# Kernel optimization log

Measured on AMD Instinct MI355X. Metric: run time of the kernel, lower is better.

The kernel has to match this reference:

```python
import jax, jax.numpy as jnp
import numpy as np

B, S, C, H, F = 4, 2048, 256, 8, 512  # scenes, pillars/scene, embed, heads, ffn hidden
D = C // H


def setup_inputs() -> dict:
    key = jax.random.key(0)
    ks = jax.random.split(key, 6)
    n = lambda k, sh: jax.random.normal(k, sh, jnp.float32) * 0.02
    # batch index sorted, equal-size contiguous segments per scene
    bidx = (jnp.arange(B * S, dtype=jnp.int32) // S)[:, None]
    coords = jnp.concatenate([bidx, jnp.zeros((B * S, 3), jnp.int32)], axis=1)
    return dict(
        pillar_features=jax.random.normal(ks[0], (B * S, C), jnp.float32),
        voxel_coords=coords,
        w_qkv=n(ks[1], (3 * C, C)), b_qkv=jnp.zeros((3 * C,), jnp.float32),
        w_out=n(ks[2], (C, C)), b_out=jnp.zeros((C,), jnp.float32),
        ln1_g=jnp.ones((C,), jnp.float32), ln1_b=jnp.zeros((C,), jnp.float32),
        w1=n(ks[3], (F, C)), b1=jnp.zeros((F,), jnp.float32),
        w2=n(ks[4], (C, F)), b2=jnp.zeros((C,), jnp.float32),
        ln2_g=jnp.ones((C,), jnp.float32), ln2_b=jnp.zeros((C,), jnp.float32),
    )


def _ln(x, g, b):
    m = x.mean(-1, keepdims=True)
    v = x.var(-1, keepdims=True)  # biased var, matches torch LayerNorm
    return (x - m) / jnp.sqrt(v + 1e-5) * g + b


def reference(pillar_features, voxel_coords, w_qkv, b_qkv, w_out, b_out,
              ln1_g, ln1_b, w1, b1, w2, b2, ln2_g, ln2_b):
    # coords[:,0] is sorted with equal-size contiguous segments, so the
    # per-batch mask-gather in the original is exactly a reshape here.
    x = pillar_features.reshape(B, S, C)
    qkv = x @ w_qkv.T + b_qkv                      # [B,S,3C]
    q, k, v = jnp.split(qkv, 3, axis=-1)
    rs = lambda t: t.reshape(B, S, H, D).transpose(0, 2, 1, 3)  # [B,H,S,D]
    q, k, v = rs(q), rs(k), rs(v)
    scores = jnp.einsum('bhqd,bhkd->bhqk', q, k) / jnp.sqrt(jnp.float32(D))
    att = jax.nn.softmax(scores, axis=-1)
    o = jnp.einsum('bhqk,bhkd->bhqd', att, v).transpose(0, 2, 1, 3).reshape(B, S, C)
    o = o @ w_out.T + b_out
    x = _ln(x + o, ln1_g, ln1_b)
    f = jax.nn.gelu(x @ w1.T + b1, approximate=False) @ w2.T + b2
    x = _ln(x + f, ln2_g, ln2_b)
    return x.reshape(B * S, C)
```

## Files before the change

kernel.cpp:

```cpp
#include <hip/hip_runtime.h>
#include <math.h>

#define MROWS 8192
#define BATCH 4
#define SEQ   2048
#define CDIM  256
#define HEADS 8
#define DHEAD 32
#define FDIM  512
#define QKVN  768

typedef __attribute__((ext_vector_type(8))) short bf16x8;
typedef __attribute__((ext_vector_type(4))) float f32x4;

__device__ __forceinline__ unsigned pk_bf16(float a, float b) {
  unsigned r;
  asm("v_cvt_pk_bf16_f32 %0, %1, %2" : "=v"(r) : "v"(a), "v"(b));
  return r;
}
__device__ __forceinline__ float bf2f(short s) {
  unsigned u = ((unsigned)(unsigned short)s) << 16;
  return __builtin_bit_cast(float, u);
}
__device__ __forceinline__ float bflo(unsigned w) {
  return __builtin_bit_cast(float, w << 16);
}
__device__ __forceinline__ float bfhi(unsigned w) {
  return __builtin_bit_cast(float, w & 0xffff0000u);
}
__device__ __forceinline__ short f2bf(float f) {
  unsigned u = __builtin_bit_cast(unsigned, f);
  u = (u + 0x7FFFu + ((u >> 16) & 1u)) >> 16;
  return (short)u;
}
__device__ __forceinline__ float fexp2(float x) {
#if __has_builtin(__builtin_amdgcn_exp2f)
  return __builtin_amdgcn_exp2f(x);
#else
  return exp2f(x);
#endif
}
__device__ __forceinline__ void gl16(const void* g, void* l) {
  __builtin_amdgcn_global_load_lds(
      (const __attribute__((address_space(1))) void*)g,
      (__attribute__((address_space(3))) void*)l, 16, 0, 0);
}
__device__ __forceinline__ float gelu_tanh(float v) {
  const float u = v * (0.7978845608f + 0.0356774081f * v * v);
  const float t = fexp2(u * 2.885390082f);
  return v * t / (t + 1.0f);
}

__global__ __launch_bounds__(256) void cast_all_k(
    const float* __restrict__ pillar, short* __restrict__ pb,
    const float* __restrict__ wq, short* __restrict__ wqb,
    const float* __restrict__ wo, short* __restrict__ wob,
    const float* __restrict__ w1, short* __restrict__ w1b,
    const float* __restrict__ w2, short* __restrict__ w2b)
{
  const int i = blockIdx.x * 256 + threadIdx.x;
  const float* s; short* d; int off;
  if (i < 524288)      { s = pillar; d = pb;  off = i; }
  else if (i < 573440) { s = wq;     d = wqb; off = i - 524288; }
  else if (i < 589824) { s = wo;     d = wob; off = i - 573440; }
  else if (i < 622592) { s = w1;     d = w1b; off = i - 589824; }
  else                 { s = w2;     d = w2b; off = i - 622592; }
  float4 v = reinterpret_cast<const float4*>(s)[off];
  uint2 o = { pk_bf16(v.x, v.y), pk_bf16(v.z, v.w) };
  *reinterpret_cast<uint2*>(d + off*4) = o;
}

template<int K, bool BF16OUT, bool GELU, bool VOUT>
__global__ __launch_bounds__(256) void gemm64_k(
    const short* __restrict__ A, const short* __restrict__ W,
    const float* __restrict__ bias, void* __restrict__ out,
    short* __restrict__ vt, int NS)
{
  __shared__ short AS[2][4096];
  __shared__ short WS[2][4096];
  const int tid = threadIdx.x;
  const int l   = tid & 63;
  const int w   = tid >> 6;
  const int m0 = blockIdx.x * 64;
  const int n0 = blockIdx.y * 64;
  const int wr = (w >> 1) * 32;
  const int wc = (w & 1) * 32;
  const int lr = l & 15;
  const int lg = l >> 4;

  f32x4 acc[2][2];
#pragma unroll
  for (int i = 0; i < 2; ++i)
#pragma unroll
    for (int j = 0; j < 2; ++j) acc[i][j] = (f32x4){0.f,0.f,0.f,0.f};

  auto stage = [&](int buf, int k0) {
#pragma unroll
    for (int i = 0; i < 2; ++i) {
      const int c = i*256 + tid;
      const int r = c >> 3;
      const int s = (c & 7) ^ (r & 7);
      gl16(A + (size_t)(m0 + r)*K + k0 + s*8, &AS[buf][c*8]);
      gl16(W + (size_t)(n0 + r)*K + k0 + s*8, &WS[buf][c*8]);
    }
  };

  stage(0, 0);
  const int NST = K / 64;
  for (int t = 0; t < NST; ++t) {
    const int buf = t & 1;
    __syncthreads();
    if (t + 1 < NST) stage(buf ^ 1, (t+1)*64);
#pragma unroll
    for (int ks = 0; ks < 2; ++ks) {
      const int sl = ((ks*4 + lg) ^ (lr & 7)) << 3;
      bf16x8 a[2], b[2];
#pragma unroll
      for (int mi = 0; mi < 2; ++mi)
        a[mi] = *reinterpret_cast<const bf16x8*>(&AS[buf][(wr + mi*16 + lr)*64 + sl]);
#pragma unroll
      for (int nj = 0; nj < 2; ++nj)
        b[nj] = *reinterpret_cast<const bf16x8*>(&WS[buf][(wc + nj*16 + lr)*64 + sl]);
#pragma unroll
      for (int mi = 0; mi < 2; ++mi)
#pragma unroll
        for (int nj = 0; nj < 2; ++nj)
          acc[mi][nj] = __builtin_amdgcn_mfma_f32_16x16x32_bf16(b[nj], a[mi], acc[mi][nj], 0, 0, 0);
    }
  }

#pragma unroll
  for (int mi = 0; mi < 2; ++mi) {
    const size_t m = m0 + wr + mi*16 + lr;
#pragma unroll
    for (int nj = 0; nj < 2; ++nj) {
      const int nf = n0 + wc + nj*16 + lg*4;
      float4 bs = *reinterpret_cast<const float4*>(&bias[nf]);
      f32x4 v = acc[mi][nj];
      float v0 = v[0]+bs.x, v1 = v[1]+bs.y, v2 = v[2]+bs.z, v3 = v[3]+bs.w;
      if (GELU) { v0 = gelu_tanh(v0); v1 = gelu_tanh(v1); v2 = gelu_tanh(v2); v3 = gelu_tanh(v3); }
      if (VOUT && n0 >= 512) {
        const int nl = nf - 512;
        const int hh = nl >> 5, dvb = nl & 31;
        const int bb = (int)(m >> 11), ss = (int)(m & 2047);
        short* vp = vt + ((size_t)((bb*8 + hh)*32 + dvb))*2048 + ss;
        vp[0] = f2bf(v0); vp[2048] = f2bf(v1); vp[4096] = f2bf(v2); vp[6144] = f2bf(v3);
      } else if (BF16OUT) {
        uint2 p = { pk_bf16(v0, v1), pk_bf16(v2, v3) };
        *reinterpret_cast<uint2*>((short*)out + m*NS + nf) = p;
      } else {
        float4 p = { v0, v1, v2, v3 };
        *reinterpret_cast<float4*>((float*)out + m*NS + nf) = p;
      }
    }
  }
}

__global__ __launch_bounds__(512, 8) void attn_mfma_k(
    const short* __restrict__ qk, const short* __restrict__ vtg,
    short* __restrict__ attno)
{
  __shared__ short KS[2][2][2048];
  __shared__ short VS[2][2][2048];

  const int tid  = threadIdx.x;
  const int lane = tid & 63;
  const int wv   = tid >> 6;
  const int st   = wv >> 2;
  const int qw   = wv & 3;
  const int bh   = blockIdx.y;
  const int b    = bh >> 3, h = bh & 7;
  const int q0   = blockIdx.x * 64 + qw * 16;

  const int lr = lane & 15;
  const int lg = lane >> 4;

  bf16x8 qf;
  {
    bf16x8 qraw = *reinterpret_cast<const bf16x8*>(
        qk + (size_t)(b*SEQ + q0 + lr)*512 + h*DHEAD + lg*8);
    const float c = 0.25508134f;
#pragma unroll
    for (int j = 0; j < 8; ++j) qf[j] = f2bf(bf2f(qraw[j]) * c);
  }
  bf16x8 ones;
#pragma unroll
  for (int j = 0; j < 8; ++j) ones[j] = (short)0x3F80;

  f32x4 o0 = {0.f,0.f,0.f,0.f}, o1 = {0.f,0.f,0.f,0.f};
  f32x4 lacc = {0.f,0.f,0.f,0.f};

  const int t256 = tid & 255;
  const short* kSrc;
  {
    const int r = t256 >> 2, s = t256 & 3;
    const int rr = r & 31;
    const int key = ((rr >> 2) & 3)*8 + ((rr >> 4) & 1)*4 + (rr & 3) + (r & 32);
    const int slog = s ^ ((r >> 1) & 3);
    kSrc = qk + (size_t)(b*SEQ + st*1024 + key)*512 + 256 + h*DHEAD + slog*8;
  }
  const short* vSrc;
  {
    const int r = t256 >> 3, s = t256 & 7;
    const int slog = s ^ (r & 7);
    vSrc = vtg + ((size_t)(bh*32 + r))*2048 + st*1024 + slog*8;
  }

  gl16(kSrc, &KS[st][0][t256*8]);
  gl16(vSrc, &VS[st][0][t256*8]);
  kSrc += 64*512; vSrc += 64;

  const int kxor = (lr >> 1) & 3;
  const int vxor = lr & 7;

  for (int t = 0; t < 16; ++t) {
    const int buf = t & 1;
    __syncthreads();
    if (t + 1 < 16) {
      gl16(kSrc, &KS[st][buf^1][t256*8]);
      gl16(vSrc, &VS[st][buf^1][t256*8]);
      kSrc += 64*512; vSrc += 64;
    }

#pragma unroll
    for (int half = 0; half < 2; ++half) {
      const int krow = (half*32 + lr)*32 + ((lg ^ kxor) << 3);
      bf16x8 kf0 = *reinterpret_cast<const bf16x8*>(&KS[st][buf][krow]);
      bf16x8 kf1 = *reinterpret_cast<const bf16x8*>(&KS[st][buf][krow + 512]);
      f32x4 z = {0.f,0.f,0.f,0.f};
      f32x4 s0 = __builtin_amdgcn_mfma_f32_16x16x32_bf16(kf0, qf, z, 0, 0, 0);
      f32x4 s1 = __builtin_amdgcn_mfma_f32_16x16x32_bf16(kf1, qf, z, 0, 0, 0);

      const int vcol = (((half*4 + lg) ^ vxor) << 3);
      bf16x8 vf0 = *reinterpret_cast<const bf16x8*>(&VS[st][buf][lr*64 + vcol]);
      bf16x8 vf1 = *reinterpret_cast<const bf16x8*>(&VS[st][buf][(lr+16)*64 + vcol]);

      float p0 = fexp2(s0[0]), p1 = fexp2(s0[1]), p2 = fexp2(s0[2]), p3 = fexp2(s0[3]);
      float p4 = fexp2(s1[0]), p5 = fexp2(s1[1]), p6 = fexp2(s1[2]), p7 = fexp2(s1[3]);
      union { bf16x8 v; unsigned w[4]; } pfu;
      pfu.w[0] = pk_bf16(p0, p1); pfu.w[1] = pk_bf16(p2, p3);
      pfu.w[2] = pk_bf16(p4, p5); pfu.w[3] = pk_bf16(p6, p7);

      o0   = __builtin_amdgcn_mfma_f32_16x16x32_bf16(vf0, pfu.v, o0, 0, 0, 0);
      o1   = __builtin_amdgcn_mfma_f32_16x16x32_bf16(vf1, pfu.v, o1, 0, 0, 0);
      lacc = __builtin_amdgcn_mfma_f32_16x16x32_bf16(ones, pfu.v, lacc, 0, 0, 0);
    }
  }

  __syncthreads();
  float* mg = (float*)&KS[0][0][0];
  const int mi = (qw*64 + lane)*10;
  if (st == 1) {
    mg[mi+0]=o0[0]; mg[mi+1]=o0[1]; mg[mi+2]=o0[2]; mg[mi+3]=o0[3];
    mg[mi+4]=o1[0]; mg[mi+5]=o1[1]; mg[mi+6]=o1[2]; mg[mi+7]=o1[3];
    mg[mi+8]=lacc[0];
  }
  __syncthreads();
  if (st == 0) {
    const float inv = 1.f / (lacc[0] + mg[mi+8]);
    float a0 = (o0[0]+mg[mi+0])*inv, a1 = (o0[1]+mg[mi+1])*inv;
    float a2 = (o0[2]+mg[mi+2])*inv, a3 = (o0[3]+mg[mi+3])*inv;
    float b0 = (o1[0]+mg[mi+4])*inv, b1 = (o1[1]+mg[mi+5])*inv;
    float b2 = (o1[2]+mg[mi+6])*inv, b3 = (o1[3]+mg[mi+7])*inv;
    short* op = attno + (size_t)(b*SEQ + q0 + lr)*CDIM + h*DHEAD;
    uint2 r0 = { pk_bf16(a0, a1), pk_bf16(a2, a3) };
    uint2 r1 = { pk_bf16(b0, b1), pk_bf16(b2, b3) };
    *reinterpret_cast<uint2*>(op + lg*4)      = r0;
    *reinterpret_cast<uint2*>(op + 16 + lg*4) = r1;
  }
}

template<int K, bool F32OUT>
__global__ __launch_bounds__(512, 4) void gemmln_k(
    const short* __restrict__ A, const short* __restrict__ W,
    const float* __restrict__ bias, const short* __restrict__ resid,
    const float* __restrict__ g, const float* __restrict__ bta,
    float* __restrict__ outf, short* __restrict__ outb)
{
  __shared__ short AS[2][2048];
  __shared__ short WS[2][16384];
  __shared__ float P[32][4][2];
  const int tid = threadIdx.x;
  const int l   = tid & 63;
  const int wv  = tid >> 6;
  const int wm  = wv >> 2;
  const int wn  = wv & 3;
  const int m0  = blockIdx.x * 32;
  const int lr  = l & 15;
  const int lg  = l >> 4;

  f32x4 acc[4];
#pragma unroll
  for (int j = 0; j < 4; ++j) acc[j] = (f32x4){0.f,0.f,0.f,0.f};

  auto stage = [&](int buf, int k0) {
    if (tid < 256) {
      const int r = tid >> 3;
      const int s = (tid & 7) ^ (r & 7);
      gl16(A + (size_t)(m0 + r)*K + k0 + s*8, &AS[buf][tid*8]);
    }
#pragma unroll
    for (int i = 0; i < 4; ++i) {
      const int c = i*512 + tid;
      const int r = c >> 3;
      const int s = (c & 7) ^ (r & 7);
      gl16(W + (size_t)r*K + k0 + s*8, &WS[buf][c*8]);
    }
  };

  stage(0, 0);
  const int NST = K / 64;
  for (int t = 0; t < NST; ++t) {
    const int buf = t & 1;
    __syncthreads();
    if (t + 1 < NST) stage(buf ^ 1, (t+1)*64);
#pragma unroll
    for (int ks = 0; ks < 2; ++ks) {
      const int sl = ((ks*4 + lg) ^ (lr & 7)) << 3;
      bf16x8 a = *reinterpret_cast<const bf16x8*>(&AS[buf][(wm*16 + lr)*64 + sl]);
#pragma unroll
      for (int nj = 0; nj < 4; ++nj) {
        bf16x8 b = *reinterpret_cast<const bf16x8*>(&WS[buf][(wn*64 + nj*16 + lr)*64 + sl]);
        acc[nj] = __builtin_amdgcn_mfma_f32_16x16x32_bf16(b, a, acc[nj], 0, 0, 0);
      }
    }
  }

  const int m = m0 + wm*16 + lr;
  float vals[16];
  float s = 0.f, sq = 0.f;
#pragma unroll
  for (int nj = 0; nj < 4; ++nj) {
    const int col = wn*64 + nj*16 + lg*4;
    float4 bs = *reinterpret_cast<const float4*>(&bias[col]);
    uint2 rv = *reinterpret_cast<const uint2*>(&resid[(size_t)m*CDIM + col]);
    float v0 = acc[nj][0] + bs.x + bflo(rv.x);
    float v1 = acc[nj][1] + bs.y + bfhi(rv.x);
    float v2 = acc[nj][2] + bs.z + bflo(rv.y);
    float v3 = acc[nj][3] + bs.w + bfhi(rv.y);
    vals[nj*4+0]=v0; vals[nj*4+1]=v1; vals[nj*4+2]=v2; vals[nj*4+3]=v3;
    s += (v0+v1)+(v2+v3);
    sq += (v0*v0+v1*v1)+(v2*v2+v3*v3);
  }
  s  += __shfl_xor(s, 16);  s  += __shfl_xor(s, 32);
  sq += __shfl_xor(sq, 16); sq += __shfl_xor(sq, 32);
  if (lg == 0) { P[wm*16 + lr][wn][0] = s; P[wm*16 + lr][wn][1] = sq; }
  __syncthreads();
  const float S  = P[wm*16+lr][0][0] + P[wm*16+lr][1][0] + P[wm*16+lr][2][0] + P[wm*16+lr][3][0];
  const float SQ = P[wm*16+lr][0][1] + P[wm*16+lr][1][1] + P[wm*16+lr][2][1] + P[wm*16+lr][3][1];
  const float mean = S * (1.f/CDIM);
  const float var  = SQ * (1.f/CDIM) - mean*mean;
  const float rstd = rsqrtf(var + 1e-5f);
#pragma unroll
  for (int nj = 0; nj < 4; ++nj) {
    const int col = wn*64 + nj*16 + lg*4;
    float4 gv = *reinterpret_cast<const float4*>(&g[col]);
    float4 bv = *reinterpret_cast<const float4*>(&bta[col]);
    float r0 = (vals[nj*4+0]-mean)*rstd*gv.x + bv.x;
    float r1 = (vals[nj*4+1]-mean)*rstd*gv.y + bv.y;
    float r2 = (vals[nj*4+2]-mean)*rstd*gv.z + bv.z;
    float r3 = (vals[nj*4+3]-mean)*rstd*gv.w + bv.w;
    if (F32OUT) {
      float4 p = { r0, r1, r2, r3 };
      *reinterpret_cast<float4*>(&outf[(size_t)m*CDIM + col]) = p;
    } else {
      uint2 p = { pk_bf16(r0, r1), pk_bf16(r2, r3) };
      *reinterpret_cast<uint2*>(outb + (size_t)m*CDIM + col) = p;
    }
  }
}

extern "C" void kernel_launch(void* const* d_in, const int* in_sizes, int n_in,
                              void* d_out, int out_size, void* d_ws, size_t ws_size,
                              hipStream_t stream)
{
  const float* pillar = (const float*)d_in[0];
  const float* w_qkv  = (const float*)d_in[2];
  const float* b_qkv  = (const float*)d_in[3];
  const float* w_out  = (const float*)d_in[4];
  const float* b_out  = (const float*)d_in[5];
  const float* ln1_g  = (const float*)d_in[6];
  const float* ln1_b  = (const float*)d_in[7];
  const float* w1     = (const float*)d_in[8];
  const float* b1     = (const float*)d_in[9];
  const float* w2     = (const float*)d_in[10];
  const float* b2     = (const float*)d_in[11];
  const float* ln2_g  = (const float*)d_in[12];
  const float* ln2_b  = (const float*)d_in[13];
  float* out = (float*)d_out;
  short* sb  = (short*)d_ws;

  short* pb    = sb;
  short* wqb   = sb + 2097152;
  short* wob   = sb + 2293760;
  short* w1b   = sb + 2359296;
  short* w2b   = sb + 2490368;
  short* qk    = sb + 2621440;
  short* vtg   = sb + 6815744;
  short* attnb = sb + 8912896;
  short* x1b   = sb + 2621440;
  short* yhidb = sb + 4718592;

  cast_all_k<<<2560, 256, 0, stream>>>(pillar, pb, w_qkv, wqb, w_out, wob,
                                       w1, w1b, w2, w2b);

  gemm64_k<CDIM, true, false, true><<<dim3(MROWS/64, QKVN/64), 256, 0, stream>>>(
      pb, wqb, b_qkv, qk, vtg, 512);

  attn_mfma_k<<<dim3(SEQ/64, BATCH*HEADS), 512, 0, stream>>>(qk, vtg, attnb);

  gemmln_k<CDIM, false><<<dim3(MROWS/32), 512, 0, stream>>>(
      attnb, wob, b_out, pb, ln1_g, ln1_b, nullptr, x1b);

  gemm64_k<CDIM, true, true, false><<<dim3(MROWS/64, FDIM/64), 256, 0, stream>>>(
      x1b, w1b, b1, yhidb, nullptr, FDIM);

  gemmln_k<FDIM, true><<<dim3(MROWS/32), 512, 0, stream>>>(
      yhidb, w2b, b2, x1b, ln2_g, ln2_b, out, nullptr);
}
```

Before: 83.08 us.

## Process two 16-query tiles per wave in attention to reuse K/V fragments

Each attention wave now handles 32 queries as two 16-row tiles instead of one, so every K and V fragment read from shared memory feeds twice as many MFMAs. The grid is halved to SEQ/128 blocks per head and the launch-bounds occupancy hint drops from 8 to 4. The goal is less LDS and global K/V traffic per query and better MFMA density. In exchange it uses more registers, halves the block count to 512, and adds an extra merge round with barriers in the epilogue.

```diff
diff --git a/kernel.cpp b/kernel.cpp
--- a/kernel.cpp
+++ b/kernel.cpp
@@ -156,7 +156,7 @@
   }
 }
 
-__global__ __launch_bounds__(512, 8) void attn_mfma_k(
+__global__ __launch_bounds__(512, 4) void attn_mfma_k(
     const short* __restrict__ qk, const short* __restrict__ vtg,
     short* __restrict__ attno)
 {
@@ -170,25 +170,31 @@
   const int qw   = wv & 3;
   const int bh   = blockIdx.y;
   const int b    = bh >> 3, h = bh & 7;
-  const int q0   = blockIdx.x * 64 + qw * 16;
+  const int q0   = blockIdx.x * 128 + qw * 32;
 
   const int lr = lane & 15;
   const int lg = lane >> 4;
 
-  bf16x8 qf;
+  bf16x8 qfa, qfb;
   {
-    bf16x8 qraw = *reinterpret_cast<const bf16x8*>(
+    const float c = 0.25508134f;
+    bf16x8 ra = *reinterpret_cast<const bf16x8*>(
         qk + (size_t)(b*SEQ + q0 + lr)*512 + h*DHEAD + lg*8);
-    const float c = 0.25508134f;
-#pragma unroll
-    for (int j = 0; j < 8; ++j) qf[j] = f2bf(bf2f(qraw[j]) * c);
+    bf16x8 rb = *reinterpret_cast<const bf16x8*>(
+        qk + (size_t)(b*SEQ + q0 + 16 + lr)*512 + h*DHEAD + lg*8);
+#pragma unroll
+    for (int j = 0; j < 8; ++j) {
+      qfa[j] = f2bf(bf2f(ra[j]) * c);
+      qfb[j] = f2bf(bf2f(rb[j]) * c);
+    }
   }
   bf16x8 ones;
 #pragma unroll
   for (int j = 0; j < 8; ++j) ones[j] = (short)0x3F80;
 
-  f32x4 o0 = {0.f,0.f,0.f,0.f}, o1 = {0.f,0.f,0.f,0.f};
-  f32x4 lacc = {0.f,0.f,0.f,0.f};
+  f32x4 oa0 = {0.f,0.f,0.f,0.f}, oa1 = {0.f,0.f,0.f,0.f};
+  f32x4 ob0 = {0.f,0.f,0.f,0.f}, ob1 = {0.f,0.f,0.f,0.f};
+  f32x4 la  = {0.f,0.f,0.f,0.f}, lb  = {0.f,0.f,0.f,0.f};
 
   const int t256 = tid & 255;
   const short* kSrc;
@@ -227,42 +233,75 @@
       const int krow = (half*32 + lr)*32 + ((lg ^ kxor) << 3);
       bf16x8 kf0 = *reinterpret_cast<const bf16x8*>(&KS[st][buf][krow]);
       bf16x8 kf1 = *reinterpret_cast<const bf16x8*>(&KS[st][buf][krow + 512]);
-      f32x4 z = {0.f,0.f,0.f,0.f};
-      f32x4 s0 = __builtin_amdgcn_mfma_f32_16x16x32_bf16(kf0, qf, z, 0, 0, 0);
-      f32x4 s1 = __builtin_amdgcn_mfma_f32_16x16x32_bf16(kf1, qf, z, 0, 0, 0);
-
       const int vcol = (((half*4 + lg) ^ vxor) << 3);
       bf16x8 vf0 = *reinterpret_cast<const bf16x8*>(&VS[st][buf][lr*64 + vcol]);
       bf16x8 vf1 = *reinterpret_cast<const bf16x8*>(&VS[st][buf][(lr+16)*64 + vcol]);
-
-      float p0 = fexp2(s0[0]), p1 = fexp2(s0[1]), p2 = fexp2(s0[2]), p3 = fexp2(s0[3]);
-      float p4 = fexp2(s1[0]), p5 = fexp2(s1[1]), p6 = fexp2(s1[2]), p7 = fexp2(s1[3]);
-      union { bf16x8 v; unsigned w[4]; } pfu;
-      pfu.w[0] = pk_bf16(p0, p1); pfu.w[1] = pk_bf16(p2, p3);
-      pfu.w[2] = pk_bf16(p4, p5); pfu.w[3] = pk_bf16(p6, p7);
-
-      o0   = __builtin_amdgcn_mfma_f32_16x16x32_bf16(vf0, pfu.v, o0, 0, 0, 0);
-      o1   = __builtin_amdgcn_mfma_f32_16x16x32_bf16(vf1, pfu.v, o1, 0, 0, 0);
-      lacc = __builtin_amdgcn_mfma_f32_16x16x32_bf16(ones, pfu.v, lacc, 0, 0, 0);
-    }
-  }
-
-  __syncthreads();
+      f32x4 z = {0.f,0.f,0.f,0.f};
+
+      {
+        f32x4 s0 = __builtin_amdgcn_mfma_f32_16x16x32_bf16(kf0, qfa, z, 0, 0, 0);
+        f32x4 s1 = __builtin_amdgcn_mfma_f32_16x16x32_bf16(kf1, qfa, z, 0, 0, 0);
+        float p0 = fexp2(s0[0]), p1 = fexp2(s0[1]), p2 = fexp2(s0[2]), p3 = fexp2(s0[3]);
+        float p4 = fexp2(s1[0]), p5 = fexp2(s1[1]), p6 = fexp2(s1[2]), p7 = fexp2(s1[3]);
+        union { bf16x8 v; unsigned w[4]; } pfu;
+        pfu.w[0] = pk_bf16(p0, p1); pfu.w[1] = pk_bf16(p2, p3);
+        pfu.w[2] = pk_bf16(p4, p5); pfu.w[3] = pk_bf16(p6, p7);
+        oa0 = __builtin_amdgcn_mfma_f32_16x16x32_bf16(vf0, pfu.v, oa0, 0, 0, 0);
+        oa1 = __builtin_amdgcn_mfma_f32_16x16x32_bf16(vf1, pfu.v, oa1, 0, 0, 0);
+        la  = __builtin_amdgcn_mfma_f32_16x16x32_bf16(ones, pfu.v, la, 0, 0, 0);
+      }
+      {
+        f32x4 s0 = __builtin_amdgcn_mfma_f32_16x16x32_bf16(kf0, qfb, z, 0, 0, 0);
+        f32x4 s1 = __builtin_amdgcn_mfma_f32_16x16x32_bf16(kf1, qfb, z, 0, 0, 0);
+        float p0 = fexp2(s0[0]), p1 = fexp2(s0[1]), p2 = fexp2(s0[2]), p3 = fexp2(s0[3]);
+        float p4 = fexp2(s1[0]), p5 = fexp2(s1[1]), p6 = fexp2(s1[2]), p7 = fexp2(s1[3]);
+        union { bf16x8 v; unsigned w[4]; } pfu;
+        pfu.w[0] = pk_bf16(p0, p1); pfu.w[1] = pk_bf16(p2, p3);
+        pfu.w[2] = pk_bf16(p4, p5); pfu.w[3] = pk_bf16(p6, p7);
+        ob0 = __builtin_amdgcn_mfma_f32_16x16x32_bf16(vf0, pfu.v, ob0, 0, 0, 0);
+        ob1 = __builtin_amdgcn_mfma_f32_16x16x32_bf16(vf1, pfu.v, ob1, 0, 0, 0);
+        lb  = __builtin_amdgcn_mfma_f32_16x16x32_bf16(ones, pfu.v, lb, 0, 0, 0);
+      }
+    }
+  }
+
   float* mg = (float*)&KS[0][0][0];
   const int mi = (qw*64 + lane)*10;
+
+  __syncthreads();
   if (st == 1) {
-    mg[mi+0]=o0[0]; mg[mi+1]=o0[1]; mg[mi+2]=o0[2]; mg[mi+3]=o0[3];
-    mg[mi+4]=o1[0]; mg[mi+5]=o1[1]; mg[mi+6]=o1[2]; mg[mi+7]=o1[3];
-    mg[mi+8]=lacc[0];
+    mg[mi+0]=oa0[0]; mg[mi+1]=oa0[1]; mg[mi+2]=oa0[2]; mg[mi+3]=oa0[3];
+    mg[mi+4]=oa1[0]; mg[mi+5]=oa1[1]; mg[mi+6]=oa1[2]; mg[mi+7]=oa1[3];
+    mg[mi+8]=la[0];
   }
   __syncthreads();
   if (st == 0) {
-    const float inv = 1.f / (lacc[0] + mg[mi+8]);
-    float a0 = (o0[0]+mg[mi+0])*inv, a1 = (o0[1]+mg[mi+1])*inv;
-    float a2 = (o0[2]+mg[mi+2])*inv, a3 = (o0[3]+mg[mi+3])*inv;
-    float b0 = (o1[0]+mg[mi+4])*inv, b1 = (o1[1]+mg[mi+5])*inv;
-    float b2 = (o1[2]+mg[mi+6])*inv, b3 = (o1[3]+mg[mi+7])*inv;
+    const float inv = 1.f / (la[0] + mg[mi+8]);
+    float a0 = (oa0[0]+mg[mi+0])*inv, a1 = (oa0[1]+mg[mi+1])*inv;
+    float a2 = (oa0[2]+mg[mi+2])*inv, a3 = (oa0[3]+mg[mi+3])*inv;
+    float b0 = (oa1[0]+mg[mi+4])*inv, b1 = (oa1[1]+mg[mi+5])*inv;
+    float b2 = (oa1[2]+mg[mi+6])*inv, b3 = (oa1[3]+mg[mi+7])*inv;
     short* op = attno + (size_t)(b*SEQ + q0 + lr)*CDIM + h*DHEAD;
+    uint2 r0 = { pk_bf16(a0, a1), pk_bf16(a2, a3) };
+    uint2 r1 = { pk_bf16(b0, b1), pk_bf16(b2, b3) };
+    *reinterpret_cast<uint2*>(op + lg*4)      = r0;
+    *reinterpret_cast<uint2*>(op + 16 + lg*4) = r1;
+  }
+
+  __syncthreads();
+  if (st == 1) {
+    mg[mi+0]=ob0[0]; mg[mi+1]=ob0[1]; mg[mi+2]=ob0[2]; mg[mi+3]=ob0[3];
+    mg[mi+4]=ob1[0]; mg[mi+5]=ob1[1]; mg[mi+6]=ob1[2]; mg[mi+7]=ob1[3];
+    mg[mi+8]=lb[0];
+  }
+  __syncthreads();
+  if (st == 0) {
+    const float inv = 1.f / (lb[0] + mg[mi+8]);
+    float a0 = (ob0[0]+mg[mi+0])*inv, a1 = (ob0[1]+mg[mi+1])*inv;
+    float a2 = (ob0[2]+mg[mi+2])*inv, a3 = (ob0[3]+mg[mi+3])*inv;
+    float b0 = (ob1[0]+mg[mi+4])*inv, b1 = (ob1[1]+mg[mi+5])*inv;
+    float b2 = (ob1[2]+mg[mi+6])*inv, b3 = (ob1[3]+mg[mi+7])*inv;
+    short* op = attno + (size_t)(b*SEQ + q0 + 16 + lr)*CDIM + h*DHEAD;
     uint2 r0 = { pk_bf16(a0, a1), pk_bf16(a2, a3) };
     uint2 r1 = { pk_bf16(b0, b1), pk_bf16(b2, b3) };
     *reinterpret_cast<uint2*>(op + lg*4)      = r0;
@@ -407,7 +446,7 @@
   gemm64_k<CDIM, true, false, true><<<dim3(MROWS/64, QKVN/64), 256, 0, stream>>>(
       pb, wqb, b_qkv, qk, vtg, 512);
 
-  attn_mfma_k<<<dim3(SEQ/64, BATCH*HEADS), 512, 0, stream>>>(qk, vtg, attnb);
+  attn_mfma_k<<<dim3(SEQ/128, BATCH*HEADS), 512, 0, stream>>>(qk, vtg, attnb);
 
   gemmln_k<CDIM, false><<<dim3(MROWS/32), 512, 0, stream>>>(
       attnb, wob, b_out, pb, ln1_g, ln1_b, nullptr, x1b);
```

After: 81.46 us. Within noise of the previous version (-1.9%).
